# Kernel optimization log

Hardware: AMD Instinct MI355X
Metric: run time of the kernel (lower is better)

Reference implementation:

```python
import jax, jax.numpy as jnp
import numpy as np

N_TOKENS = 16384
HIDDEN = 4096
N_EXPERTS = 64
TOP_K = 8


def setup_inputs() -> dict:
    key = jax.random.key(0)
    kx, kw, kb = jax.random.split(key, 3)
    x = jax.random.normal(kx, (N_TOKENS, HIDDEN), dtype=jnp.float32)
    # nn.Linear(hidden_dim, expert_num): weight [E, H], bias [E]
    W = jax.random.normal(kw, (N_EXPERTS, HIDDEN), dtype=jnp.float32) * (1.0 / np.sqrt(HIDDEN))
    b = jax.random.normal(kb, (N_EXPERTS,), dtype=jnp.float32) * 0.01
    return {"x": x, "W": W, "b": b}


def reference(x, W, b):
    # gate linear: [N, H] @ [H, E] + [E] -> [N, E]
    router = jnp.einsum("nh,eh->ne", x, W) + b
    # softmax over experts
    router_logits = jax.nn.softmax(router, axis=-1)
    # top-k over experts: values/indices [N, K]
    top_k_logits, top_k_indices = jax.lax.top_k(router_logits, TOP_K)
    # renormalize the selected probs
    router_weight = top_k_logits / jnp.sum(top_k_logits, axis=-1, keepdims=True)
    router_weight = router_weight.astype(x.dtype)
    # one-hot mask [N, K, E] -> permute(2,1,0) -> [E, K, N]
    expert_mask = jax.nn.one_hot(top_k_indices, N_EXPERTS, dtype=jnp.int32)
    expert_mask = jnp.transpose(expert_mask, (2, 1, 0))
    return (router, router_weight, top_k_indices, expert_mask)
```

## Files before the change

### kernel.cpp

```cpp
#include <hip/hip_runtime.h>

#define N_TOK 16384
#define HID   4096
#define N_EXP 64
#define TOPK  8

#define SPLIT  4
#define KSLICE (HID / SPLIT)
#define CH     32
#define NCH    (KSLICE / CH)
#define TB     128
#define XSTR   132
#define WSTR   68

#define OFF_WT   (N_TOK * N_EXP)
#define OFF_IDX  (OFF_WT + N_TOK * TOPK)
#define OFF_MASK (OFF_IDX + N_TOK * TOPK)

__global__ __launch_bounds__(256, 2)
void router_gemm(const float* __restrict__ x, const float* __restrict__ W,
                 float* __restrict__ router)
{
    __shared__ __align__(16) float xs[2][CH][XSTR];
    __shared__ __align__(16) float ws[2][CH][WSTR];

    const int tid = threadIdx.x;
    const int tb  = blockIdx.x & 127;
    const int ks  = blockIdx.x >> 7;
    const long t0 = (long)tb * TB;
    const int h0  = ks * KSLICE;

    const int lane = tid & 63;
    const int wv   = tid >> 6;
    const int trow = wv * 16 + (lane >> 4) * 4;
    const int ecol = (lane & 15) * 4;

    const int tf = tid >> 3;
    const int hq = tid & 7;

    const float* xsrc = x + (t0 + tf) * (long)HID + h0 + 4 * hq;
    const float* wsrc = W + (long)tf * HID + h0 + 4 * hq;

    float acc[8][4] = {{0.f}};
    float4 px[4], pw[2];

#pragma unroll
    for (int j = 0; j < 4; ++j) px[j] = *(const float4*)(xsrc + (long)(32 * j) * HID);
#pragma unroll
    for (int j = 0; j < 2; ++j) pw[j] = *(const float4*)(wsrc + (long)(32 * j) * HID);

#pragma unroll
    for (int jj = 0; jj < 4; ++jj) {
#pragma unroll
        for (int j = 0; j < 4; ++j) xs[0][4 * hq + jj][tf + 32 * j] = ((const float*)&px[j])[jj];
#pragma unroll
        for (int j = 0; j < 2; ++j) ws[0][4 * hq + jj][tf + 32 * j] = ((const float*)&pw[j])[jj];
    }
    __syncthreads();

    for (int c = 0; c < NCH; ++c) {
        const int buf = c & 1;

        if (c + 1 < NCH) {
#pragma unroll
            for (int j = 0; j < 4; ++j) px[j] = *(const float4*)(xsrc + (c + 1) * CH + (long)(32 * j) * HID);
#pragma unroll
            for (int j = 0; j < 2; ++j) pw[j] = *(const float4*)(wsrc + (c + 1) * CH + (long)(32 * j) * HID);
        }

#pragma unroll 4
        for (int k = 0; k < CH; ++k) {
            float4 xa = *(const float4*)&xs[buf][k][trow];
            float4 xb = *(const float4*)&xs[buf][k][trow + 64];
            float4 wq = *(const float4*)&ws[buf][k][ecol];
#pragma unroll
            for (int i = 0; i < 4; ++i) {
                float xv = ((const float*)&xa)[i];
                acc[i][0] = fmaf(xv, wq.x, acc[i][0]);
                acc[i][1] = fmaf(xv, wq.y, acc[i][1]);
                acc[i][2] = fmaf(xv, wq.z, acc[i][2]);
                acc[i][3] = fmaf(xv, wq.w, acc[i][3]);
            }
#pragma unroll
            for (int i = 0; i < 4; ++i) {
                float xv = ((const float*)&xb)[i];
                acc[4 + i][0] = fmaf(xv, wq.x, acc[4 + i][0]);
                acc[4 + i][1] = fmaf(xv, wq.y, acc[4 + i][1]);
                acc[4 + i][2] = fmaf(xv, wq.z, acc[4 + i][2]);
                acc[4 + i][3] = fmaf(xv, wq.w, acc[4 + i][3]);
            }
        }

        if (c + 1 < NCH) {
            const int nb = buf ^ 1;
#pragma unroll
            for (int jj = 0; jj < 4; ++jj) {
#pragma unroll
                for (int j = 0; j < 4; ++j) xs[nb][4 * hq + jj][tf + 32 * j] = ((const float*)&px[j])[jj];
#pragma unroll
                for (int j = 0; j < 2; ++j) ws[nb][4 * hq + jj][tf + 32 * j] = ((const float*)&pw[j])[jj];
            }
        }
        __syncthreads();
    }

#pragma unroll
    for (int h = 0; h < 2; ++h) {
        float* rbase = router + (t0 + trow + 64 * h) * (long)N_EXP + ecol;
#pragma unroll
        for (int i = 0; i < 4; ++i)
#pragma unroll
            for (int j = 0; j < 4; ++j)
                unsafeAtomicAdd(rbase + (long)i * N_EXP + j, acc[4 * h + i][j]);
    }
}

__global__ __launch_bounds__(256)
void router_topk(float* __restrict__ router, const float* __restrict__ b,
                 float* __restrict__ out)
{
    const int tid  = threadIdx.x;
    const int lane = tid & 63;
    const int wv   = tid >> 6;
    const int n    = blockIdx.x * 4 + wv;

    float l = router[(long)n * N_EXP + lane] + b[lane];
    router[(long)n * N_EXP + lane] = l;

    float m = l;
#pragma unroll
    for (int o = 32; o > 0; o >>= 1) m = fmaxf(m, __shfl_xor(m, o));
    float p = expf(l - m);
    float Z = p;
#pragma unroll
    for (int o = 32; o > 0; o >>= 1) Z += __shfl_xor(Z, o);
    float prob = p / Z;

    float cur = prob;
    float myv = 0.f;
    int   myi = 0;
    float ssum = 0.f;
#pragma unroll
    for (int k = 0; k < TOPK; ++k) {
        float v = cur;
        int   id = lane;
#pragma unroll
        for (int o = 32; o > 0; o >>= 1) {
            float ov = __shfl_xor(v, o);
            int   oi = __shfl_xor(id, o);
            if (ov > v || (ov == v && oi < id)) { v = ov; id = oi; }
        }
        if (lane == k)  { myv = v; myi = id; }
        if (lane == id) cur = -1.f;
        ssum += v;
    }

    if (lane < TOPK) {
        out[OFF_WT  + (long)n * TOPK + lane] = myv / ssum;
        out[OFF_IDX + (long)n * TOPK + lane] = (float)myi;
    }
}

__global__ __launch_bounds__(256)
void mask_fill(const float* __restrict__ idxf, float* __restrict__ mask)
{
    const int k  = blockIdx.x >> 4;
    const int n0 = ((blockIdx.x & 15) * 256 + threadIdx.x) * 4;

    int sel[4];
#pragma unroll
    for (int t = 0; t < 4; ++t)
        sel[t] = (int)idxf[(long)(n0 + t) * TOPK + k];

#pragma unroll 8
    for (int e = 0; e < N_EXP; ++e) {
        float4 v;
        v.x = (sel[0] == e) ? 1.0f : 0.0f;
        v.y = (sel[1] == e) ? 1.0f : 0.0f;
        v.z = (sel[2] == e) ? 1.0f : 0.0f;
        v.w = (sel[3] == e) ? 1.0f : 0.0f;
        *(float4*)(mask + (long)(e * TOPK + k) * N_TOK + n0) = v;
    }
}

extern "C" void kernel_launch(void* const* d_in, const int* in_sizes, int n_in,
                              void* d_out, int out_size, void* d_ws, size_t ws_size,
                              hipStream_t stream)
{
    const float* x = (const float*)d_in[0];
    const float* W = (const float*)d_in[1];
    const float* b = (const float*)d_in[2];
    float* out = (float*)d_out;

    hipMemsetAsync(out, 0, (size_t)(N_TOK * N_EXP) * sizeof(float), stream);

    hipLaunchKernelGGL(router_gemm, dim3(TB * SPLIT == 512 ? 512 : 512), dim3(256), 0, stream,
                       x, W, out);
    hipLaunchKernelGGL(router_topk, dim3(N_TOK / 4), dim3(256), 0, stream,
                       out, b, out);
    hipLaunchKernelGGL(mask_fill, dim3(128), dim3(256), 0, stream,
                       out + OFF_IDX, out + OFF_MASK);
}
```

Baseline: 475.7 us.

## Replace FP32 FMA router GEMM with split-bf16 MFMA emulation

Replaces the shared-memory-tiled FP32 FMA GEMM with a matrix-core kernel. Each fp32 operand is split into three bf16 parts (high, mid, low) and six bf16 MFMA products are summed to approximate fp32 accuracy. W is pre-split once per call by a new kernel into workspace, while x is split in registers and fed straight from global memory with no LDS staging. This trades extra conversion ALU work and six MFMAs per tile for matrix-core throughput, and accuracy now depends on the dropped cross terms, which may shift near-tied top-k choices.

```diff
diff --git a/kernel.cpp b/kernel.cpp
--- a/kernel.cpp
+++ b/kernel.cpp
@@ -5,114 +5,159 @@
 #define N_EXP 64
 #define TOPK  8
 
-#define SPLIT  4
-#define KSLICE (HID / SPLIT)
-#define CH     32
-#define NCH    (KSLICE / CH)
-#define TB     128
-#define XSTR   132
-#define WSTR   68
+#define SPLIT 4
+#define KS    (HID / SPLIT)
+#define TBLK  128
 
 #define OFF_WT   (N_TOK * N_EXP)
 #define OFF_IDX  (OFF_WT + N_TOK * TOPK)
 #define OFF_MASK (OFF_IDX + N_TOK * TOPK)
 
+typedef __attribute__((ext_vector_type(8))) short bf16x8;
+typedef __attribute__((ext_vector_type(4))) float f32x4;
+
+__device__ __forceinline__ unsigned short f2bf(float f) {
+    unsigned u = __float_as_uint(f);
+    u += 0x7FFFu + ((u >> 16) & 1u);
+    return (unsigned short)(u >> 16);
+}
+__device__ __forceinline__ float bf2f(unsigned short h) {
+    return __uint_as_float((unsigned)h << 16);
+}
+
+__global__ __launch_bounds__(256)
+void wconv(const float* __restrict__ W, unsigned short* __restrict__ Wh,
+           unsigned short* __restrict__ Wm, unsigned short* __restrict__ Wl)
+{
+    const int i = (blockIdx.x * 256 + threadIdx.x) * 4;
+    float4 w = *(const float4*)(W + i);
+    ushort4 h, m, l;
+#pragma unroll
+    for (int j = 0; j < 4; ++j) {
+        float v = ((const float*)&w)[j];
+        unsigned short hh = f2bf(v); float r1 = v - bf2f(hh);
+        unsigned short mm = f2bf(r1); float r2 = r1 - bf2f(mm);
+        unsigned short ll = f2bf(r2);
+        ((unsigned short*)&h)[j] = hh;
+        ((unsigned short*)&m)[j] = mm;
+        ((unsigned short*)&l)[j] = ll;
+    }
+    *(ushort4*)(Wh + i) = h;
+    *(ushort4*)(Wm + i) = m;
+    *(ushort4*)(Wl + i) = l;
+}
+
 __global__ __launch_bounds__(256, 2)
-void router_gemm(const float* __restrict__ x, const float* __restrict__ W,
+void router_mfma(const float* __restrict__ x,
+                 const unsigned short* __restrict__ Wh,
+                 const unsigned short* __restrict__ Wm,
+                 const unsigned short* __restrict__ Wl,
                  float* __restrict__ router)
 {
-    __shared__ __align__(16) float xs[2][CH][XSTR];
-    __shared__ __align__(16) float ws[2][CH][WSTR];
-
-    const int tid = threadIdx.x;
-    const int tb  = blockIdx.x & 127;
-    const int ks  = blockIdx.x >> 7;
-    const long t0 = (long)tb * TB;
-    const int h0  = ks * KSLICE;
-
+    const int tid  = threadIdx.x;
     const int lane = tid & 63;
     const int wv   = tid >> 6;
-    const int trow = wv * 16 + (lane >> 4) * 4;
-    const int ecol = (lane & 15) * 4;
-
-    const int tf = tid >> 3;
-    const int hq = tid & 7;
-
-    const float* xsrc = x + (t0 + tf) * (long)HID + h0 + 4 * hq;
-    const float* wsrc = W + (long)tf * HID + h0 + 4 * hq;
-
-    float acc[8][4] = {{0.f}};
-    float4 px[4], pw[2];
-
-#pragma unroll
-    for (int j = 0; j < 4; ++j) px[j] = *(const float4*)(xsrc + (long)(32 * j) * HID);
-#pragma unroll
-    for (int j = 0; j < 2; ++j) pw[j] = *(const float4*)(wsrc + (long)(32 * j) * HID);
-
-#pragma unroll
-    for (int jj = 0; jj < 4; ++jj) {
-#pragma unroll
-        for (int j = 0; j < 4; ++j) xs[0][4 * hq + jj][tf + 32 * j] = ((const float*)&px[j])[jj];
-#pragma unroll
-        for (int j = 0; j < 2; ++j) ws[0][4 * hq + jj][tf + 32 * j] = ((const float*)&pw[j])[jj];
-    }
-    __syncthreads();
-
-    for (int c = 0; c < NCH; ++c) {
-        const int buf = c & 1;
-
-        if (c + 1 < NCH) {
-#pragma unroll
-            for (int j = 0; j < 4; ++j) px[j] = *(const float4*)(xsrc + (c + 1) * CH + (long)(32 * j) * HID);
-#pragma unroll
-            for (int j = 0; j < 2; ++j) pw[j] = *(const float4*)(wsrc + (c + 1) * CH + (long)(32 * j) * HID);
-        }
-
-#pragma unroll 4
-        for (int k = 0; k < CH; ++k) {
-            float4 xa = *(const float4*)&xs[buf][k][trow];
-            float4 xb = *(const float4*)&xs[buf][k][trow + 64];
-            float4 wq = *(const float4*)&ws[buf][k][ecol];
-#pragma unroll
-            for (int i = 0; i < 4; ++i) {
-                float xv = ((const float*)&xa)[i];
-                acc[i][0] = fmaf(xv, wq.x, acc[i][0]);
-                acc[i][1] = fmaf(xv, wq.y, acc[i][1]);
-                acc[i][2] = fmaf(xv, wq.z, acc[i][2]);
-                acc[i][3] = fmaf(xv, wq.w, acc[i][3]);
+    const int tb   = blockIdx.x & 127;
+    const int ksl  = blockIdx.x >> 7;
+    const int m16  = lane & 15;
+    const int quad = lane >> 4;
+    const long t0  = (long)tb * TBLK + wv * 32;
+    const int kb   = ksl * KS + quad * 8;
+
+    f32x4 acc[2][4];
+#pragma unroll
+    for (int a = 0; a < 2; ++a)
+#pragma unroll
+        for (int n = 0; n < 4; ++n) acc[a][n] = (f32x4){0.f, 0.f, 0.f, 0.f};
+
+    const float* xp0 = x + (t0 + m16) * (long)HID + kb;
+    const float* xp1 = x + (t0 + 16 + m16) * (long)HID + kb;
+    const unsigned short* wh = Wh + (long)m16 * HID + kb;
+    const unsigned short* wm = Wm + (long)m16 * HID + kb;
+    const unsigned short* wl = Wl + (long)m16 * HID + kb;
+
+    float4 nx[4];
+    nx[0] = *(const float4*)(xp0);
+    nx[1] = *(const float4*)(xp0 + 4);
+    nx[2] = *(const float4*)(xp1);
+    nx[3] = *(const float4*)(xp1 + 4);
+
+    for (int k = 0; k < KS; k += 32) {
+        float4 cx[4];
+#pragma unroll
+        for (int j = 0; j < 4; ++j) cx[j] = nx[j];
+        if (k + 32 < KS) {
+            nx[0] = *(const float4*)(xp0 + k + 32);
+            nx[1] = *(const float4*)(xp0 + k + 36);
+            nx[2] = *(const float4*)(xp1 + k + 32);
+            nx[3] = *(const float4*)(xp1 + k + 36);
+        }
+
+        bf16x8 Bh[4], Bm[4], Bl[4];
+#pragma unroll
+        for (int n = 0; n < 4; ++n) {
+            const long wo = (long)(n * 16) * HID + k;
+            Bh[n] = *(const bf16x8*)(wh + wo);
+            Bm[n] = *(const bf16x8*)(wm + wo);
+            Bl[n] = *(const bf16x8*)(wl + wo);
+        }
+
+        bf16x8 Ah[2], Am[2], Al[2];
+#pragma unroll
+        for (int mt = 0; mt < 2; ++mt) {
+            const float* p = (const float*)&cx[2 * mt];
+#pragma unroll
+            for (int j = 0; j < 8; ++j) {
+                float v = p[j];
+                unsigned short hh = f2bf(v); float r1 = v - bf2f(hh);
+                unsigned short mm = f2bf(r1); float r2 = r1 - bf2f(mm);
+                unsigned short ll = f2bf(r2);
+                Ah[mt][j] = (short)hh; Am[mt][j] = (short)mm; Al[mt][j] = (short)ll;
             }
-#pragma unroll
-            for (int i = 0; i < 4; ++i) {
-                float xv = ((const float*)&xb)[i];
-                acc[4 + i][0] = fmaf(xv, wq.x, acc[4 + i][0]);
-                acc[4 + i][1] = fmaf(xv, wq.y, acc[4 + i][1]);
-                acc[4 + i][2] = fmaf(xv, wq.z, acc[4 + i][2]);
-                acc[4 + i][3] = fmaf(xv, wq.w, acc[4 + i][3]);
+        }
+
+#pragma unroll
+        for (int n = 0; n < 4; ++n)
+#pragma unroll
+            for (int mt = 0; mt < 2; ++mt)
+                acc[mt][n] = __builtin_amdgcn_mfma_f32_16x16x32_bf16(Ah[mt], Bh[n], acc[mt][n], 0, 0, 0);
+#pragma unroll
+        for (int n = 0; n < 4; ++n)
+#pragma unroll
+            for (int mt = 0; mt < 2; ++mt)
+                acc[mt][n] = __builtin_amdgcn_mfma_f32_16x16x32_bf16(Ah[mt], Bm[n], acc[mt][n], 0, 0, 0);
+#pragma unroll
+        for (int n = 0; n < 4; ++n)
+#pragma unroll
+            for (int mt = 0; mt < 2; ++mt)
+                acc[mt][n] = __builtin_amdgcn_mfma_f32_16x16x32_bf16(Am[mt], Bh[n], acc[mt][n], 0, 0, 0);
+#pragma unroll
+        for (int n = 0; n < 4; ++n)
+#pragma unroll
+            for (int mt = 0; mt < 2; ++mt)
+                acc[mt][n] = __builtin_amdgcn_mfma_f32_16x16x32_bf16(Ah[mt], Bl[n], acc[mt][n], 0, 0, 0);
+#pragma unroll
+        for (int n = 0; n < 4; ++n)
+#pragma unroll
+            for (int mt = 0; mt < 2; ++mt)
+                acc[mt][n] = __builtin_amdgcn_mfma_f32_16x16x32_bf16(Al[mt], Bh[n], acc[mt][n], 0, 0, 0);
+#pragma unroll
+        for (int n = 0; n < 4; ++n)
+#pragma unroll
+            for (int mt = 0; mt < 2; ++mt)
+                acc[mt][n] = __builtin_amdgcn_mfma_f32_16x16x32_bf16(Am[mt], Bm[n], acc[mt][n], 0, 0, 0);
+    }
+
+#pragma unroll
+    for (int mt = 0; mt < 2; ++mt)
+#pragma unroll
+        for (int n = 0; n < 4; ++n)
+#pragma unroll
+            for (int r = 0; r < 4; ++r) {
+                long tok = t0 + mt * 16 + quad * 4 + r;
+                int  e   = n * 16 + m16;
+                unsafeAtomicAdd(router + tok * (long)N_EXP + e, acc[mt][n][r]);
             }
-        }
-
-        if (c + 1 < NCH) {
-            const int nb = buf ^ 1;
-#pragma unroll
-            for (int jj = 0; jj < 4; ++jj) {
-#pragma unroll
-                for (int j = 0; j < 4; ++j) xs[nb][4 * hq + jj][tf + 32 * j] = ((const float*)&px[j])[jj];
-#pragma unroll
-                for (int j = 0; j < 2; ++j) ws[nb][4 * hq + jj][tf + 32 * j] = ((const float*)&pw[j])[jj];
-            }
-        }
-        __syncthreads();
-    }
-
-#pragma unroll
-    for (int h = 0; h < 2; ++h) {
-        float* rbase = router + (t0 + trow + 64 * h) * (long)N_EXP + ecol;
-#pragma unroll
-        for (int i = 0; i < 4; ++i)
-#pragma unroll
-            for (int j = 0; j < 4; ++j)
-                unsafeAtomicAdd(rbase + (long)i * N_EXP + j, acc[4 * h + i][j]);
-    }
 }
 
 __global__ __launch_bounds__(256)
@@ -192,10 +237,16 @@
     const float* b = (const float*)d_in[2];
     float* out = (float*)d_out;
 
+    unsigned short* Wh = (unsigned short*)d_ws;
+    unsigned short* Wm = Wh + (size_t)N_EXP * HID;
+    unsigned short* Wl = Wm + (size_t)N_EXP * HID;
+
     hipMemsetAsync(out, 0, (size_t)(N_TOK * N_EXP) * sizeof(float), stream);
 
-    hipLaunchKernelGGL(router_gemm, dim3(TB * SPLIT == 512 ? 512 : 512), dim3(256), 0, stream,
-                       x, W, out);
+    hipLaunchKernelGGL(wconv, dim3(N_EXP * HID / 1024), dim3(256), 0, stream,
+                       W, Wh, Wm, Wl);
+    hipLaunchKernelGGL(router_mfma, dim3(128 * SPLIT), dim3(256), 0, stream,
+                       x, Wh, Wm, Wl, out);
     hipLaunchKernelGGL(router_topk, dim3(N_TOK / 4), dim3(256), 0, stream,
                        out, b, out);
     hipLaunchKernelGGL(mask_fill, dim3(128), dim3(256), 0, stream,
```

After: 478.1 us. About the same (+0.5%).
